# Kernel tuning notes

Hardware: AMD Instinct MI355X
Metric: run time of the kernel (lower is better)

The kernel has to match this reference:

```python
import jax, jax.numpy as jnp
import numpy as np

NUM_LANDMARKS = 256
PINV_ITERS = 6


def iterative_inv(K):
    # Newton-Schulz iterative pseudo-inverse (Nystromformer), K: [B, m, m]
    I = jnp.eye(K.shape[-1], dtype=K.dtype)
    V = K.swapaxes(-1, -2) / (jnp.max(jnp.sum(K, axis=-2)) * jnp.max(jnp.sum(K, axis=-1)))
    for _ in range(PINV_ITERS):
        KV = K @ V
        V = 0.25 * V @ (13.0 * I - KV @ (15.0 * I - KV @ (7.0 * I - KV)))
    return V


def nystrom_attention_matrix(q, k, m):
    # q, k: [B, N, d] -> approximate softmax(q k^T / sqrt(d)) of shape [B, N, N]
    B, N, d = q.shape
    scale = 1.0 / jnp.sqrt(jnp.asarray(d, q.dtype))
    L = N // m
    q_l = q.reshape(B, m, L, d).mean(axis=2)  # landmark queries [B, m, d]
    k_l = k.reshape(B, m, L, d).mean(axis=2)  # landmark keys    [B, m, d]
    k1 = jax.nn.softmax(jnp.einsum('bnd,bmd->bnm', q, k_l) * scale, axis=-1)   # [B, N, m]
    k2 = jax.nn.softmax(jnp.einsum('bld,bmd->blm', q_l, k_l) * scale, axis=-1) # [B, m, m]
    k3 = jax.nn.softmax(jnp.einsum('bmd,bnd->bmn', q_l, k) * scale, axis=-1)   # [B, m, N]
    return (k1 @ iterative_inv(k2)) @ k3  # [B, N, N]


def setup_inputs() -> dict:
    key = jax.random.key(0)
    ks = jax.random.split(key, 8)
    B, C, T, W, H = 2, 64, 4, 32, 32
    d = C // 8
    scale = 0.05  # keep q.k scores in a sane softmax range
    return {
        'x': jax.random.normal(ks[0], (B, C, T, W, H), dtype=jnp.float32),
        'wq': jax.random.normal(ks[1], (d, C), dtype=jnp.float32) * scale,
        'bq': jax.random.normal(ks[2], (d,), dtype=jnp.float32) * scale,
        'wk': jax.random.normal(ks[3], (d, C), dtype=jnp.float32) * scale,
        'bk': jax.random.normal(ks[4], (d,), dtype=jnp.float32) * scale,
        'wv': jax.random.normal(ks[5], (C, C), dtype=jnp.float32) * scale,
        'bv': jax.random.normal(ks[6], (C,), dtype=jnp.float32) * scale,
        'gamma': jax.random.normal(ks[7], (1,), dtype=jnp.float32),
    }


def reference(x, wq, bq, wk, bk, wv, bv, gamma):
    B, C, T, W, H = x.shape
    N = T * W * H
    xf = x.reshape(B, C, N)
    # 1x1x1 Conv3d == per-token linear over channels
    q = jnp.einsum('oc,bcn->bno', wq, xf) + bq            # [B, N, C//8]
    k = jnp.einsum('oc,bcn->bno', wk, xf) + bk            # [B, N, C//8]
    v = jnp.einsum('oc,bcn->bon', wv, xf) + bv[None, :, None]  # [B, C, N]
    attn = nystrom_attention_matrix(q, k, NUM_LANDMARKS)  # [B, N, N]
    # out = bmm(value, attn^T): out[b,c,i] = sum_j v[b,c,j] * attn[b,i,j]
    out = jnp.einsum('bcj,bij->bci', v, attn).reshape(B, C, T, W, H)
    out = gamma[0] * out + x
    return out, attn
```

## Files before the change

### kernel.cpp

```cpp
#include <hip/hip_runtime.h>
#include <hip/hip_bf16.h>
#include <math.h>

#define NB 2
#define NC 64
#define ND 8
#define NN 4096
#define NM 256
#define NL 16
#define SCALE 0.35355339059327373f
#define PS (NB * NM * NM)

typedef __attribute__((ext_vector_type(4))) float f32x4;
typedef __attribute__((ext_vector_type(8))) short bf16x8;

__device__ inline ushort f2bf(float f) {
  __hip_bfloat16 h = __float2bfloat16(f);
  return *reinterpret_cast<ushort*>(&h);
}
__device__ inline float bf2f(ushort u) {
  return __uint_as_float(((unsigned int)u) << 16);
}

__device__ inline void gl_lds16(const void* g, void* l) {
  __builtin_amdgcn_global_load_lds(
      (const __attribute__((address_space(1))) unsigned int*)g,
      (__attribute__((address_space(3))) unsigned int*)l, 16, 0, 0);
}

__global__ __launch_bounds__(256) void qkv2l_kernel(
    const float* __restrict__ x,
    const float* __restrict__ wq, const float* __restrict__ bq,
    const float* __restrict__ wk, const float* __restrict__ bk,
    const float* __restrict__ wv, const float* __restrict__ bv,
    float* __restrict__ q, float* __restrict__ k, float* __restrict__ v,
    float* __restrict__ ql, float* __restrict__ kl) {
  __shared__ float ws[NC];
  int o = blockIdx.x;
  int b = blockIdx.z;
  int n0 = blockIdx.y * 1024;
  int t = threadIdx.x;
  const float* wrow;
  float bias;
  if (o < ND)            { wrow = wq + (size_t)o * NC;            bias = bq[o]; }
  else if (o < 2 * ND)   { wrow = wk + (size_t)(o - ND) * NC;     bias = bk[o - ND]; }
  else                   { wrow = wv + (size_t)(o - 2 * ND) * NC; bias = bv[o - 2 * ND]; }
  if (t < NC) ws[t] = wrow[t];
  __syncthreads();
  int n = n0 + t * 4;
  float4 acc = {bias, bias, bias, bias};
  #pragma unroll
  for (int c = 0; c < NC; ++c) {
    float wc = ws[c];
    float4 xv = *(const float4*)(x + ((size_t)b * NC + c) * NN + n);
    acc.x += wc * xv.x; acc.y += wc * xv.y; acc.z += wc * xv.z; acc.w += wc * xv.w;
  }
  if (o < ND) {
    float* qp = q + ((size_t)b * NN + n) * ND + o;
    qp[0] = acc.x; qp[8] = acc.y; qp[16] = acc.z; qp[24] = acc.w;
  } else if (o < 2 * ND) {
    float* kp = k + ((size_t)b * NN + n) * ND + (o - ND);
    kp[0] = acc.x; kp[8] = acc.y; kp[16] = acc.z; kp[24] = acc.w;
  } else {
    *(float4*)(v + ((size_t)b * NC + (o - 2 * ND)) * NN + n) = acc;
  }
  if (o < 2 * ND) {
    float s4 = acc.x + acc.y + acc.z + acc.w;
    s4 += __shfl_xor(s4, 1);
    s4 += __shfl_xor(s4, 2);
    if ((t & 3) == 0) {
      int g = n0 / 16 + (t >> 2);
      float* dst = (o < ND) ? ql : kl;
      dst[((size_t)b * NM + g) * ND + (o & 7)] = s4 * (1.0f / 16.0f);
    }
  }
}

__global__ __launch_bounds__(256) void scores_all_kernel(
    const float* __restrict__ q, const float* __restrict__ ql,
    const float* __restrict__ kw, const float* __restrict__ kl,
    ushort* __restrict__ k1bf, float* __restrict__ k2w,
    float* __restrict__ k3w, float* __restrict__ kvw) {
  __shared__ float skl[NM][9];
  __shared__ float wred[4], wsum[4];
  int blk = blockIdx.x;
  int t = threadIdx.x;
  if (blk < 2048 + 128) {
    const float* Q; int R, b, xrow;
    bool isbf;
    if (blk < 2048) { b = blk >> 10; xrow = blk & 1023; Q = q;  R = NN; isbf = true; }
    else { int r = blk - 2048; b = r >> 6; xrow = r & 63; Q = ql; R = NM; isbf = false; }
    for (int i = t; i < NM * ND; i += 256) skl[i >> 3][i & 7] = kl[(size_t)b * NM * ND + i];
    __syncthreads();
    int wave = t >> 6, lane = t & 63;
    int r = xrow * 4 + wave;
    const float* qrow = Q + ((size_t)b * R + r) * ND;
    float qr[ND];
    #pragma unroll
    for (int dd = 0; dd < ND; ++dd) qr[dd] = qrow[dd];
    float sc[4];
    float lmax = -1e30f;
    #pragma unroll
    for (int s = 0; s < 4; ++s) {
      int j = lane + 64 * s;
      float a = 0.f;
      #pragma unroll
      for (int dd = 0; dd < ND; ++dd) a += qr[dd] * skl[j][dd];
      sc[s] = a * SCALE;
      lmax = fmaxf(lmax, sc[s]);
    }
    for (int off = 32; off; off >>= 1) lmax = fmaxf(lmax, __shfl_xor(lmax, off));
    float lsum = 0.f;
    #pragma unroll
    for (int s = 0; s < 4; ++s) { sc[s] = expf(sc[s] - lmax); lsum += sc[s]; }
    for (int off = 32; off; off >>= 1) lsum += __shfl_xor(lsum, off);
    float inv = 1.0f / lsum;
    if (isbf) {
      #pragma unroll
      for (int s = 0; s < 4; ++s)
        k1bf[((size_t)b * R + r) * NM + lane + 64 * s] = f2bf(sc[s] * inv);
    } else {
      #pragma unroll
      for (int s = 0; s < 4; ++s)
        k2w[((size_t)b * R + r) * NM + lane + 64 * s] = sc[s] * inv;
    }
  } else if (blk < 2048 + 128 + 512) {
    int r = blk - 2176;
    int b = r >> 8, i = r & 255;
    float qr[ND];
    #pragma unroll
    for (int dd = 0; dd < ND; ++dd) qr[dd] = ql[((size_t)b * NM + i) * ND + dd];
    float sc[16];
    float lmax = -1e30f;
    #pragma unroll
    for (int s = 0; s < 16; ++s) {
      int n = t + 256 * s;
      const float* kp = kw + ((size_t)b * NN + n) * ND;
      float a = 0.f;
      #pragma unroll
      for (int dd = 0; dd < ND; ++dd) a += qr[dd] * kp[dd];
      sc[s] = a * SCALE;
      lmax = fmaxf(lmax, sc[s]);
    }
    for (int off = 32; off; off >>= 1) lmax = fmaxf(lmax, __shfl_xor(lmax, off));
    if ((t & 63) == 0) wred[t >> 6] = lmax;
    __syncthreads();
    lmax = fmaxf(fmaxf(wred[0], wred[1]), fmaxf(wred[2], wred[3]));
    float lsum = 0.f;
    #pragma unroll
    for (int s = 0; s < 16; ++s) { sc[s] = expf(sc[s] - lmax); lsum += sc[s]; }
    for (int off = 32; off; off >>= 1) lsum += __shfl_xor(lsum, off);
    if ((t & 63) == 0) wsum[t >> 6] = lsum;
    __syncthreads();
    lsum = wsum[0] + wsum[1] + wsum[2] + wsum[3];
    float inv = 1.0f / lsum;
    #pragma unroll
    for (int s = 0; s < 16; ++s) k3w[((size_t)b * NM + i) * NN + t + 256 * s] = sc[s] * inv;
  } else {
    int r = blk - 2688;
    kvw[r * 256 + t] = 0.0f;
  }
}

__global__ __launch_bounds__(256) void denom_k3t_kernel(
    const float* __restrict__ k2, float* __restrict__ denw,
    const float* __restrict__ k3, ushort* __restrict__ k3t) {
  __shared__ float red[256];
  __shared__ float tile[32][33];
  int blk = blockIdx.x;
  int t = threadIdx.x;
  if (blk < NB) {
    int b = blk;
    float cs = 0.f;
    for (int i = 0; i < NM; ++i) cs += k2[((size_t)b * NM + i) * NM + t];
    red[t] = cs;
    __syncthreads();
    for (int off = 128; off; off >>= 1) {
      if (t < off) red[t] = fmaxf(red[t], red[t + off]);
      __syncthreads();
    }
    if (t == 0) denw[b] = red[0];
  } else {
    int r = blk - NB;
    int n0 = (r & 127) * 32, m0 = ((r >> 7) & 7) * 32, b = r >> 10;
    int rr = t >> 3, c4 = (t & 7) * 4;
    float4 v = *(const float4*)(k3 + ((size_t)b * NM + m0 + rr) * NN + n0 + c4);
    tile[c4][rr] = v.x; tile[c4 + 1][rr] = v.y; tile[c4 + 2][rr] = v.z; tile[c4 + 3][rr] = v.w;
    __syncthreads();
    ushort4 u;
    u.x = f2bf(tile[rr][c4]);     u.y = f2bf(tile[rr][c4 + 1]);
    u.z = f2bf(tile[rr][c4 + 2]); u.w = f2bf(tile[rr][c4 + 3]);
    *(ushort4*)(k3t + ((size_t)b * NN + n0 + rr) * NM + m0 + c4) = u;
  }
}

__global__ __launch_bounds__(64) void ns_gemm(
    const float* __restrict__ A, int amode,
    const float* __restrict__ B, int bmode,
    const float* __restrict__ denw, float* __restrict__ O,
    float s_a, float s_ab) {
  __shared__ float As[128][36];
  __shared__ float Bs[128][36];
  int t = threadIdx.x;
  int bj = blockIdx.x * 32, bi = blockIdx.y * 32;
  int b = blockIdx.z >> 1, slice = blockIdx.z & 1;
  int k0 = slice * 128;
  size_t bo = (size_t)b * NM * NM;
  float dval = (amode == 2 || bmode == 2) ? 1.0f / fmaxf(denw[0], denw[1]) : 0.f;
  {
    int r = t >> 1, kc0 = (t & 1) * 64;
    if (amode == 2) {
      for (int i = 0; i < 64; ++i) {
        int kk = kc0 + i;
        As[kk][r] = A[bo + (size_t)(k0 + kk) * NM + bi + r] * dval;
      }
    } else if (amode == 1) {
      for (int i = 0; i < 16; ++i) {
        const float* p = A + bo + (size_t)(bi + r) * NM + k0 + kc0 + i * 4;
        float4 v0 = *(const float4*)p;
        float4 v1 = *(const float4*)(p + PS);
        As[kc0 + i * 4 + 0][r] = v0.x + v1.x;
        As[kc0 + i * 4 + 1][r] = v0.y + v1.y;
        As[kc0 + i * 4 + 2][r] = v0.z + v1.z;
        As[kc0 + i * 4 + 3][r] = v0.w + v1.w;
      }
    } else {
      for (int i = 0; i < 16; ++i) {
        float4 v0 = *(const float4*)(A + bo + (size_t)(bi + r) * NM + k0 + kc0 + i * 4);
        As[kc0 + i * 4 + 0][r] = v0.x;
        As[kc0 + i * 4 + 1][r] = v0.y;
        As[kc0 + i * 4 + 2][r] = v0.z;
        As[kc0 + i * 4 + 3][r] = v0.w;
      }
    }
    if (bmode == 2) {
      for (int i2 = 0; i2 < 2; ++i2) {
        int kr = t + 64 * i2;
        for (int c = 0; c < 32; ++c)
          Bs[kr][c] = B[bo + (size_t)(bj + c) * NM + k0 + kr] * dval;
      }
    } else if (bmode == 1) {
      for (int i2 = 0; i2 < 2; ++i2) {
        int kr = t + 64 * i2;
        for (int c4 = 0; c4 < 32; c4 += 4) {
          const float* p = B + bo + (size_t)(k0 + kr) * NM + bj + c4;
          float4 v0 = *(const float4*)p;
          float4 v1 = *(const float4*)(p + PS);
          v0.x += v1.x; v0.y += v1.y; v0.z += v1.z; v0.w += v1.w;
          *(float4*)&Bs[kr][c4] = v0;
        }
      }
    } else {
      for (int i2 = 0; i2 < 2; ++i2) {
        int kr = t + 64 * i2;
        for (int c4 = 0; c4 < 32; c4 += 4)
          *(float4*)&Bs[kr][c4] =
              *(const float4*)(B + bo + (size_t)(k0 + kr) * NM + bj + c4);
      }
    }
  }
  __syncthreads();
  int tx = t & 7, ty = t >> 3;
  float acc[4][4] = {};
  #pragma unroll 4
  for (int kk = 0; kk < 128; ++kk) {
    float4 a4 = *(const float4*)&As[kk][ty * 4];
    float4 b4 = *(const float4*)&Bs[kk][tx * 4];
    float av[4] = {a4.x, a4.y, a4.z, a4.w};
    float bv[4] = {b4.x, b4.y, b4.z, b4.w};
    #pragma unroll
    for (int i = 0; i < 4; ++i)
      #pragma unroll
      for (int j = 0; j < 4; ++j) acc[i][j] += av[i] * bv[j];
  }
  float* Op = O + (size_t)slice * PS + bo;
  bool addA = (slice == 0) && (s_a != 0.0f);
  #pragma unroll
  for (int i = 0; i < 4; ++i) {
    int row = bi + ty * 4 + i;
    float4 rv;
    rv.x = s_ab * acc[i][0]; rv.y = s_ab * acc[i][1];
    rv.z = s_ab * acc[i][2]; rv.w = s_ab * acc[i][3];
    if (addA) {
      int col = bj + tx * 4;
      if (amode == 2) {
        rv.x += s_a * A[bo + (size_t)(col + 0) * NM + row] * dval;
        rv.y += s_a * A[bo + (size_t)(col + 1) * NM + row] * dval;
        rv.z += s_a * A[bo + (size_t)(col + 2) * NM + row] * dval;
        rv.w += s_a * A[bo + (size_t)(col + 3) * NM + row] * dval;
      } else if (amode == 1) {
        const float* p = A + bo + (size_t)row * NM + col;
        float4 a0 = *(const float4*)p;
        float4 a1 = *(const float4*)(p + PS);
        rv.x += s_a * (a0.x + a1.x); rv.y += s_a * (a0.y + a1.y);
        rv.z += s_a * (a0.z + a1.z); rv.w += s_a * (a0.w + a1.w);
      } else {
        float4 a0 = *(const float4*)(A + bo + (size_t)row * NM + col);
        rv.x += s_a * a0.x; rv.y += s_a * a0.y;
        rv.z += s_a * a0.z; rv.w += s_a * a0.w;
      }
    }
    *(float4*)(Op + (size_t)row * NM + bj + tx * 4) = rv;
  }
}

__global__ __launch_bounds__(256) void cvt_vinv_kernel(const float* __restrict__ Vp,
                                                       ushort* __restrict__ Vt) {
  int b = blockIdx.z;
  int n0 = blockIdx.x * 32, m0 = blockIdx.y * 32;
  __shared__ float tile[32][33];
  int t = threadIdx.x;
  int r = t >> 3, c4 = (t & 7) * 4;
  size_t bo = (size_t)b * NM * NM;
  const float* p = Vp + bo + (size_t)(m0 + r) * NM + n0 + c4;
  float4 v0 = *(const float4*)p;
  float4 v1 = *(const float4*)(p + PS);
  tile[c4][r] = v0.x + v1.x; tile[c4 + 1][r] = v0.y + v1.y;
  tile[c4 + 2][r] = v0.z + v1.z; tile[c4 + 3][r] = v0.w + v1.w;
  __syncthreads();
  ushort4 u;
  u.x = f2bf(tile[r][c4]);     u.y = f2bf(tile[r][c4 + 1]);
  u.z = f2bf(tile[r][c4 + 2]); u.w = f2bf(tile[r][c4 + 3]);
  *(ushort4*)(Vt + bo + (size_t)(n0 + r) * NM + m0 + c4) = u;
}

__global__ __launch_bounds__(256) void gemm_a_mfma(
    const ushort* __restrict__ k1bf, const ushort* __restrict__ Vt,
    ushort* __restrict__ Abf) {
  int b = blockIdx.z;
  int bi = blockIdx.y * 128, bj = blockIdx.x * 128;
  __shared__ ushort As[128 * 64];
  __shared__ ushort Bs[128 * 64];
  int t = threadIdx.x;
  int wave = t >> 6, lane = t & 63;
  int wr = wave >> 1, wc = wave & 1;
  const ushort* Ab = k1bf + (size_t)b * NN * NM;
  const ushort* Bb = Vt + (size_t)b * NM * NM;
  f32x4 acc[4][4] = {};
  for (int k0 = 0; k0 < NM; k0 += 64) {
    #pragma unroll
    for (int q = 0; q < 4; ++q) {
      int s = q * 256 + t;
      int r = s >> 3, c = s & 7;
      int cs = (c ^ (r & 7)) << 3;
      gl_lds16(Ab + (size_t)(bi + r) * NM + k0 + cs, As + (size_t)s * 8);
      gl_lds16(Bb + (size_t)(bj + r) * NM + k0 + cs, Bs + (size_t)s * 8);
    }
    __syncthreads();
    #pragma unroll
    for (int kk = 0; kk < 2; ++kk) {
      int koff = kk * 64 + (lane >> 4) * 16;
      bf16x8 af[4], bfv[4];
      #pragma unroll
      for (int mi = 0; mi < 4; ++mi) {
        int row = wr * 64 + mi * 16 + (lane & 15);
        af[mi] = *(const bf16x8*)((const char*)As + row * 128 + (koff ^ ((row & 7) << 4)));
      }
      #pragma unroll
      for (int nj = 0; nj < 4; ++nj) {
        int row = wc * 64 + nj * 16 + (lane & 15);
        bfv[nj] = *(const bf16x8*)((const char*)Bs + row * 128 + (koff ^ ((row & 7) << 4)));
      }
      #pragma unroll
      for (int mi = 0; mi < 4; ++mi)
        #pragma unroll
        for (int nj = 0; nj < 4; ++nj)
          acc[mi][nj] = __builtin_amdgcn_mfma_f32_16x16x32_bf16(af[mi], bfv[nj], acc[mi][nj], 0, 0, 0);
    }
    __syncthreads();
  }
  int col = lane & 15, rbase = (lane >> 4) * 4;
  #pragma unroll
  for (int mi = 0; mi < 4; ++mi)
    #pragma unroll
    for (int nj = 0; nj < 4; ++nj)
      #pragma unroll
      for (int r = 0; r < 4; ++r)
        Abf[((size_t)b * NN + bi + wr * 64 + mi * 16 + rbase + r) * NM
            + bj + wc * 64 + nj * 16 + col] = f2bf(acc[mi][nj][r]);
}

__global__ __launch_bounds__(256) void attn_kv_kernel(
    const ushort* __restrict__ Abf, const ushort* __restrict__ K3T,
    float* __restrict__ attn, const float* __restrict__ k3w,
    const float* __restrict__ vw, float* __restrict__ kvw) {
  __shared__ char smem[32768];
  int blk = blockIdx.x;
  int t = threadIdx.x;
  if (blk < 2048) {
    ushort* As = (ushort*)smem;
    ushort* Bs = (ushort*)(smem + 16384);
    int swz = (blk & 7) * 256 + (blk >> 3);
    int b = swz >> 10;
    int rem = swz & 1023;
    int bi = (rem >> 5) * 128, bj = (rem & 31) * 128;
    int wave = t >> 6, lane = t & 63;
    int wr = wave >> 1, wc = wave & 1;
    const ushort* Ab = Abf + (size_t)b * NN * NM;
    const ushort* Bb = K3T + (size_t)b * NN * NM;
    f32x4 acc[4][4] = {};
    for (int k0 = 0; k0 < NM; k0 += 64) {
      #pragma unroll
      for (int q = 0; q < 4; ++q) {
        int s = q * 256 + t;
        int r = s >> 3, c = s & 7;
        int cs = (c ^ (r & 7)) << 3;
        gl_lds16(Ab + (size_t)(bi + r) * NM + k0 + cs, As + (size_t)s * 8);
        gl_lds16(Bb + (size_t)(bj + r) * NM + k0 + cs, Bs + (size_t)s * 8);
      }
      __syncthreads();
      #pragma unroll
      for (int kk = 0; kk < 2; ++kk) {
        int koff = kk * 64 + (lane >> 4) * 16;
        bf16x8 af[4], bfv[4];
        #pragma unroll
        for (int mi = 0; mi < 4; ++mi) {
          int row = wr * 64 + mi * 16 + (lane & 15);
          af[mi] = *(const bf16x8*)((const char*)As + row * 128 + (koff ^ ((row & 7) << 4)));
        }
        #pragma unroll
        for (int nj = 0; nj < 4; ++nj) {
          int row = wc * 64 + nj * 16 + (lane & 15);
          bfv[nj] = *(const bf16x8*)((const char*)Bs + row * 128 + (koff ^ ((row & 7) << 4)));
        }
        #pragma unroll
        for (int mi = 0; mi < 4; ++mi)
          #pragma unroll
          for (int nj = 0; nj < 4; ++nj)
            acc[mi][nj] = __builtin_amdgcn_mfma_f32_16x16x32_bf16(af[mi], bfv[nj], acc[mi][nj], 0, 0, 0);
      }
      __syncthreads();
    }
    int col = lane & 15, rbase = (lane >> 4) * 4;
    #pragma unroll
    for (int mi = 0; mi < 4; ++mi)
      #pragma unroll
      for (int nj = 0; nj < 4; ++nj)
        #pragma unroll
        for (int r = 0; r < 4; ++r)
          attn[((size_t)b * NN + bi + wr * 64 + mi * 16 + rbase + r) * NN
               + bj + wc * 64 + nj * 16 + col] = acc[mi][nj][r];
  } else {
    typedef float KVRow[33];
    KVRow* Ks = (KVRow*)smem;
    KVRow* Vs = (KVRow*)(smem + 64 * 33 * 4);
    int r = blk - 2048;
    int bp = (r & 3) * 64;
    int jsl = (r >> 2) & 31;
    int b = r >> 7;
    int j0base = jsl * (NN / 32);
    int tx = t & 15, ty = t >> 4;
    int lrow = t >> 2, ljc = (t & 3) * 8;
    float acc[4][4] = {};
    for (int j0 = j0base; j0 < j0base + NN / 32; j0 += 32) {
      float4 a0 = *(const float4*)(k3w + ((size_t)b * NM + bp + lrow) * NN + j0 + ljc);
      float4 a1 = *(const float4*)(k3w + ((size_t)b * NM + bp + lrow) * NN + j0 + ljc + 4);
      float4 v0 = *(const float4*)(vw + ((size_t)b * NC + lrow) * NN + j0 + ljc);
      float4 v1 = *(const float4*)(vw + ((size_t)b * NC + lrow) * NN + j0 + ljc + 4);
      Ks[lrow][ljc + 0] = a0.x; Ks[lrow][ljc + 1] = a0.y; Ks[lrow][ljc + 2] = a0.z; Ks[lrow][ljc + 3] = a0.w;
      Ks[lrow][ljc + 4] = a1.x; Ks[lrow][ljc + 5] = a1.y; Ks[lrow][ljc + 6] = a1.z; Ks[lrow][ljc + 7] = a1.w;
      Vs[lrow][ljc + 0] = v0.x; Vs[lrow][ljc + 1] = v0.y; Vs[lrow][ljc + 2] = v0.z; Vs[lrow][ljc + 3] = v0.w;
      Vs[lrow][ljc + 4] = v1.x; Vs[lrow][ljc + 5] = v1.y; Vs[lrow][ljc + 6] = v1.z; Vs[lrow][ljc + 7] = v1.w;
      __syncthreads();
      #pragma unroll
      for (int kk = 0; kk < 32; ++kk) {
        float av_[4], bv_[4];
        #pragma unroll
        for (int i = 0; i < 4; ++i) av_[i] = Ks[(ty << 2) + i][kk];
        #pragma unroll
        for (int j = 0; j < 4; ++j) bv_[j] = Vs[(tx << 2) + j][kk];
        #pragma unroll
        for (int i = 0; i < 4; ++i)
          #pragma unroll
          for (int j = 0; j < 4; ++j) acc[i][j] += av_[i] * bv_[j];
      }
      __syncthreads();
    }
    #pragma unroll
    for (int i = 0; i < 4; ++i)
      #pragma unroll
      for (int j = 0; j < 4; ++j)
        atomicAdd(&kvw[((size_t)b * NM + bp + (ty << 2) + i) * NC + (tx << 2) + j], acc[i][j]);
  }
}

__global__ __launch_bounds__(256) void out_kernel(
    const ushort* __restrict__ Abf, const float* __restrict__ kvm,
    const float* __restrict__ x, const float* __restrict__ gamma,
    float* __restrict__ outp) {
  __shared__ float As[32 * 256];
  int blk = blockIdx.x;
  int b = blk / (NN / 32), n0 = (blk % (NN / 32)) * 32;
  int t = threadIdx.x;
  for (int it = 0; it < 32; ++it)
    As[it * 256 + (t ^ (it & 31))] = bf2f(Abf[((size_t)b * NN + n0 + it) * NM + t]);
  __syncthreads();
  int tn = t & 31, cg0 = (t >> 5) * 8;
  float g = gamma[0];
  float acc[8] = {};
  for (int p = 0; p < NM; ++p) {
    float a = As[tn * 256 + (p ^ (tn & 31))];
    float4 kv0 = *(const float4*)(kvm + ((size_t)b * NM + p) * NC + cg0);
    float4 kv1 = *(const float4*)(kvm + ((size_t)b * NM + p) * NC + cg0 + 4);
    acc[0] += a * kv0.x; acc[1] += a * kv0.y; acc[2] += a * kv0.z; acc[3] += a * kv0.w;
    acc[4] += a * kv1.x; acc[5] += a * kv1.y; acc[6] += a * kv1.z; acc[7] += a * kv1.w;
  }
  #pragma unroll
  for (int qd = 0; qd < 8; ++qd) {
    int c = cg0 + qd;
    size_t idx = ((size_t)b * NC + c) * NN + n0 + tn;
    outp[idx] = g * acc[qd] + x[idx];
  }
}

extern "C" void kernel_launch(void* const* d_in, const int* in_sizes, int n_in,
                              void* d_out, int out_size, void* d_ws, size_t ws_size,
                              hipStream_t stream) {
  const float* x     = (const float*)d_in[0];
  const float* wq    = (const float*)d_in[1];
  const float* bq    = (const float*)d_in[2];
  const float* wk    = (const float*)d_in[3];
  const float* bk    = (const float*)d_in[4];
  const float* wv    = (const float*)d_in[5];
  const float* bv    = (const float*)d_in[6];
  const float* gamma = (const float*)d_in[7];
  float* outp = (float*)d_out;
  float* attn = outp + (size_t)NB * NC * NN;
  float* w = (float*)d_ws;

  float* qw   = w;
  float* kw   = qw + 65536;
  float* vw   = kw + 65536;
  float* qlw  = vw + 524288;
  float* klw  = qlw + 4096;
  float* k1w  = klw + 4096;
  float* k2w  = k1w + 2097152;
  float* k3w  = k2w + 131072;
  float* Abuf = k3w + 2097152;
  float* Zp   = Abuf + 1048576;
  float* T1p  = Zp + 2 * PS;
  float* T2p  = T1p + 2 * PS;
  float* Vap  = T2p + 2 * PS;
  float* Vbp  = Vap + 2 * PS;
  float* kvw  = Vbp + 2 * PS;
  float* denw = kvw + 32768;
  ushort* k1bf  = (ushort*)k1w;
  ushort* k3T   = (ushort*)k1w + 2097152;
  ushort* Abf   = (ushort*)Abuf;
  ushort* Vinvt = (ushort*)Zp;

  qkv2l_kernel<<<dim3(80, NN / 1024, NB), dim3(256), 0, stream>>>(
      x, wq, bq, wk, bk, wv, bv, qw, kw, vw, qlw, klw);
  scores_all_kernel<<<dim3(2048 + 128 + 512 + 128), dim3(256), 0, stream>>>(
      qw, qlw, kw, klw, k1bf, k2w, k3w, kvw);
  denom_k3t_kernel<<<dim3(NB + 2048), dim3(256), 0, stream>>>(k2w, denw, k3w, k3T);

  const float* Vptr = k2w; int vmode = 2;
  float* Vout = Vap;
  float* Vfin = nullptr;
  for (int it = 0; it < 6; ++it) {
    ns_gemm<<<dim3(8, 8, NB * 2), dim3(64), 0, stream>>>(k2w, 0, Vptr, vmode, denw, Zp, 0.f, 1.f);
    ns_gemm<<<dim3(8, 8, NB * 2), dim3(64), 0, stream>>>(Zp, 1, Zp, 1, denw, T1p, 7.f, -1.f);
    ns_gemm<<<dim3(8, 8, NB * 2), dim3(64), 0, stream>>>(Zp, 1, T1p, 1, denw, T2p, 15.f, -1.f);
    ns_gemm<<<dim3(8, 8, NB * 2), dim3(64), 0, stream>>>(Vptr, vmode, T2p, 1, denw, Vout, 3.25f, -0.25f);
    Vfin = Vout;
    Vptr = Vout; vmode = 1;
    Vout = (Vout == Vap) ? Vbp : Vap;
  }

  cvt_vinv_kernel<<<dim3(NM / 32, NM / 32, NB), dim3(256), 0, stream>>>(Vfin, Vinvt);
  gemm_a_mfma<<<dim3(NM / 128, NN / 128, NB), dim3(256), 0, stream>>>(k1bf, Vinvt, Abf);
  attn_kv_kernel<<<dim3(2048 + 256), dim3(256), 0, stream>>>(Abf, k3T, attn, k3w, vw, kvw);
  out_kernel<<<dim3(NB * NN / 32), dim3(256), 0, stream>>>(Abf, kvw, x, gamma, outp);
}
```

Baseline: 328.8 us.

## Refactor Newton-Schulz polynomial into three GEMMs and fuse kv/out stages

Rewrites the Newton-Schulz update polynomial 13I-15KV+7KV^2-KV^3 by factoring it with a real root. This cuts the per-iteration chain from four GEMMs to three kernels, two of them independent and batched in one launch, and drops the split-K partial-sum buffers. The final iteration writes the transposed bf16 inverse directly, which removes the separate conversion kernel. The kv = k3·v^T reduction moves into the denom/transpose kernel, so the output projection can merge into the attention kernel and one launch disappears. The factored form may change floating-point rounding, and the new GEMM tiles use 256 threads with full-K loads in place of split-K.

```diff
diff --git a/kernel.cpp b/kernel.cpp
--- a/kernel.cpp
+++ b/kernel.cpp
@@ -9,7 +9,9 @@
 #define NM 256
 #define NL 16
 #define SCALE 0.35355339059327373f
-#define PS (NB * NM * NM)
+#define A_ROOT 4.1303956f
+#define B_COEF (-2.8696044f)
+#define C_COEF 3.1474086f
 
 typedef __attribute__((ext_vector_type(4))) float f32x4;
 typedef __attribute__((ext_vector_type(8))) short bf16x8;
@@ -162,14 +164,15 @@
   }
 }
 
-__global__ __launch_bounds__(256) void denom_k3t_kernel(
+__global__ __launch_bounds__(256) void denom_k3t_kv_kernel(
     const float* __restrict__ k2, float* __restrict__ denw,
-    const float* __restrict__ k3, ushort* __restrict__ k3t) {
-  __shared__ float red[256];
-  __shared__ float tile[32][33];
+    const float* __restrict__ k3, ushort* __restrict__ k3t,
+    const float* __restrict__ vw, float* __restrict__ kvw) {
+  __shared__ char smem[34048];
   int blk = blockIdx.x;
   int t = threadIdx.x;
   if (blk < NB) {
+    float* red = (float*)smem;
     int b = blk;
     float cs = 0.f;
     for (int i = 0; i < NM; ++i) cs += k2[((size_t)b * NM + i) * NM + t];
@@ -180,7 +183,9 @@
       __syncthreads();
     }
     if (t == 0) denw[b] = red[0];
-  } else {
+  } else if (blk < NB + 2048) {
+    typedef float TRow[33];
+    TRow* tile = (TRow*)smem;
     int r = blk - NB;
     int n0 = (r & 127) * 32, m0 = ((r >> 7) & 7) * 32, b = r >> 10;
     int rr = t >> 3, c4 = (t & 7) * 4;
@@ -191,137 +196,171 @@
     u.x = f2bf(tile[rr][c4]);     u.y = f2bf(tile[rr][c4 + 1]);
     u.z = f2bf(tile[rr][c4 + 2]); u.w = f2bf(tile[rr][c4 + 3]);
     *(ushort4*)(k3t + ((size_t)b * NN + n0 + rr) * NM + m0 + c4) = u;
-  }
-}
-
-__global__ __launch_bounds__(64) void ns_gemm(
+  } else {
+    typedef float KVRow[33];
+    KVRow* Ks = (KVRow*)smem;
+    KVRow* Vs = (KVRow*)(smem + 64 * 33 * 4);
+    int r = blk - (NB + 2048);
+    int bp = (r & 3) * 64;
+    int jsl = (r >> 2) & 31;
+    int b = r >> 7;
+    int j0base = jsl * (NN / 32);
+    int tx = t & 15, ty = t >> 4;
+    int lrow = t >> 2, ljc = (t & 3) * 8;
+    float acc[4][4] = {};
+    for (int j0 = j0base; j0 < j0base + NN / 32; j0 += 32) {
+      float4 a0 = *(const float4*)(k3 + ((size_t)b * NM + bp + lrow) * NN + j0 + ljc);
+      float4 a1 = *(const float4*)(k3 + ((size_t)b * NM + bp + lrow) * NN + j0 + ljc + 4);
+      float4 v0 = *(const float4*)(vw + ((size_t)b * NC + lrow) * NN + j0 + ljc);
+      float4 v1 = *(const float4*)(vw + ((size_t)b * NC + lrow) * NN + j0 + ljc + 4);
+      Ks[lrow][ljc + 0] = a0.x; Ks[lrow][ljc + 1] = a0.y; Ks[lrow][ljc + 2] = a0.z; Ks[lrow][ljc + 3] = a0.w;
+      Ks[lrow][ljc + 4] = a1.x; Ks[lrow][ljc + 5] = a1.y; Ks[lrow][ljc + 6] = a1.z; Ks[lrow][ljc + 7] = a1.w;
+      Vs[lrow][ljc + 0] = v0.x; Vs[lrow][ljc + 1] = v0.y; Vs[lrow][ljc + 2] = v0.z; Vs[lrow][ljc + 3] = v0.w;
+      Vs[lrow][ljc + 4] = v1.x; Vs[lrow][ljc + 5] = v1.y; Vs[lrow][ljc + 6] = v1.z; Vs[lrow][ljc + 7] = v1.w;
+      __syncthreads();
+      #pragma unroll
+      for (int kk = 0; kk < 32; ++kk) {
+        float av_[4], bv_[4];
+        #pragma unroll
+        for (int i = 0; i < 4; ++i) av_[i] = Ks[(ty << 2) + i][kk];
+        #pragma unroll
+        for (int j = 0; j < 4; ++j) bv_[j] = Vs[(tx << 2) + j][kk];
+        #pragma unroll
+        for (int i = 0; i < 4; ++i)
+          #pragma unroll
+          for (int j = 0; j < 4; ++j) acc[i][j] += av_[i] * bv_[j];
+      }
+      __syncthreads();
+    }
+    #pragma unroll
+    for (int i = 0; i < 4; ++i)
+      #pragma unroll
+      for (int j = 0; j < 4; ++j)
+        atomicAdd(&kvw[((size_t)b * NM + bp + (ty << 2) + i) * NC + (tx << 2) + j], acc[i][j]);
+  }
+}
+
+__device__ __forceinline__ void ns_core(
     const float* __restrict__ A, int amode,
-    const float* __restrict__ B, int bmode,
-    const float* __restrict__ denw, float* __restrict__ O,
-    float s_a, float s_ab) {
-  __shared__ float As[128][36];
-  __shared__ float Bs[128][36];
-  int t = threadIdx.x;
-  int bj = blockIdx.x * 32, bi = blockIdx.y * 32;
-  int b = blockIdx.z >> 1, slice = blockIdx.z & 1;
-  int k0 = slice * 128;
+    const float* __restrict__ B, int bmode, const float* __restrict__ Bp,
+    float dval, float s_a, float s_ab,
+    float* __restrict__ O, ushort* __restrict__ Ot, int wmode,
+    int bi, int bj, size_t bo, float (*As)[260], float (*Bs)[36], int t) {
+  if (amode == 0) {
+    #pragma unroll
+    for (int q = 0; q < 8; ++q) {
+      int s = q * 256 + t;
+      int r = s >> 6, kc = (s & 63) * 4;
+      *(float4*)&As[r][kc] = *(const float4*)(A + bo + (size_t)(bi + r) * NM + kc);
+    }
+  } else {
+    #pragma unroll
+    for (int q = 0; q < 8; ++q) {
+      int s = q * 256 + t;
+      int k = s >> 3, rc = (s & 7) * 4;
+      float4 v = *(const float4*)(A + bo + (size_t)k * NM + bi + rc);
+      As[rc + 0][k] = v.x * dval; As[rc + 1][k] = v.y * dval;
+      As[rc + 2][k] = v.z * dval; As[rc + 3][k] = v.w * dval;
+    }
+  }
+  if (bmode == 0) {
+    #pragma unroll
+    for (int q = 0; q < 8; ++q) {
+      int s = q * 256 + t;
+      int k = s >> 3, c = (s & 7) * 4;
+      *(float4*)&Bs[k][c] = *(const float4*)(B + bo + (size_t)k * NM + bj + c);
+    }
+  } else if (bmode == 2) {
+    #pragma unroll
+    for (int q = 0; q < 8; ++q) {
+      int s = q * 256 + t;
+      int c = s >> 6, k4 = (s & 63) * 4;
+      float4 v = *(const float4*)(B + bo + (size_t)(bj + c) * NM + k4);
+      Bs[k4 + 0][c] = v.x * dval; Bs[k4 + 1][c] = v.y * dval;
+      Bs[k4 + 2][c] = v.z * dval; Bs[k4 + 3][c] = v.w * dval;
+    }
+  } else {
+    #pragma unroll
+    for (int q = 0; q < 8; ++q) {
+      int s = q * 256 + t;
+      int k = s >> 3, c = (s & 7) * 4;
+      float4 v = *(const float4*)(B + bo + (size_t)k * NM + bj + c);
+      float4 z = *(const float4*)(Bp + bo + (size_t)k * NM + bj + c);
+      float4 rr;
+      rr.x = v.x + B_COEF * z.x; rr.y = v.y + B_COEF * z.y;
+      rr.z = v.z + B_COEF * z.z; rr.w = v.w + B_COEF * z.w;
+      int d = k - bj - c;
+      if (d >= 0 && d < 4) ((float*)&rr)[d] += C_COEF;
+      *(float4*)&Bs[k][c] = rr;
+    }
+  }
+  __syncthreads();
+  int tx = t & 15, ty = t >> 4;
+  float acc[2][2] = {};
+  #pragma unroll 8
+  for (int kk = 0; kk < NM; ++kk) {
+    float a0 = As[ty * 2][kk], a1 = As[ty * 2 + 1][kk];
+    float b0 = Bs[kk][tx * 2], b1 = Bs[kk][tx * 2 + 1];
+    acc[0][0] += a0 * b0; acc[0][1] += a0 * b1;
+    acc[1][0] += a1 * b0; acc[1][1] += a1 * b1;
+  }
+  #pragma unroll
+  for (int i = 0; i < 2; ++i)
+    #pragma unroll
+    for (int j = 0; j < 2; ++j) {
+      int R = bi + ty * 2 + i, C = bj + tx * 2 + j;
+      float rv = s_ab * acc[i][j];
+      if (s_a != 0.0f) {
+        float av;
+        if (amode == 2) av = A[bo + (size_t)C * NM + R] * dval;
+        else            av = A[bo + (size_t)R * NM + C];
+        rv += s_a * av;
+      }
+      if (wmode == 0) O[bo + (size_t)R * NM + C] = rv;
+      else            Ot[bo + (size_t)C * NM + R] = f2bf(rv);
+    }
+}
+
+__global__ __launch_bounds__(256) void ns_z_kernel(
+    const float* __restrict__ k2, const float* __restrict__ V, int bmode,
+    const float* __restrict__ denw, float* __restrict__ Z) {
+  __shared__ float As[32][260];
+  __shared__ float Bs[256][36];
+  int bj = blockIdx.x * 32, bi = blockIdx.y * 32, b = blockIdx.z;
   size_t bo = (size_t)b * NM * NM;
-  float dval = (amode == 2 || bmode == 2) ? 1.0f / fmaxf(denw[0], denw[1]) : 0.f;
-  {
-    int r = t >> 1, kc0 = (t & 1) * 64;
-    if (amode == 2) {
-      for (int i = 0; i < 64; ++i) {
-        int kk = kc0 + i;
-        As[kk][r] = A[bo + (size_t)(k0 + kk) * NM + bi + r] * dval;
-      }
-    } else if (amode == 1) {
-      for (int i = 0; i < 16; ++i) {
-        const float* p = A + bo + (size_t)(bi + r) * NM + k0 + kc0 + i * 4;
-        float4 v0 = *(const float4*)p;
-        float4 v1 = *(const float4*)(p + PS);
-        As[kc0 + i * 4 + 0][r] = v0.x + v1.x;
-        As[kc0 + i * 4 + 1][r] = v0.y + v1.y;
-        As[kc0 + i * 4 + 2][r] = v0.z + v1.z;
-        As[kc0 + i * 4 + 3][r] = v0.w + v1.w;
-      }
-    } else {
-      for (int i = 0; i < 16; ++i) {
-        float4 v0 = *(const float4*)(A + bo + (size_t)(bi + r) * NM + k0 + kc0 + i * 4);
-        As[kc0 + i * 4 + 0][r] = v0.x;
-        As[kc0 + i * 4 + 1][r] = v0.y;
-        As[kc0 + i * 4 + 2][r] = v0.z;
-        As[kc0 + i * 4 + 3][r] = v0.w;
-      }
-    }
-    if (bmode == 2) {
-      for (int i2 = 0; i2 < 2; ++i2) {
-        int kr = t + 64 * i2;
-        for (int c = 0; c < 32; ++c)
-          Bs[kr][c] = B[bo + (size_t)(bj + c) * NM + k0 + kr] * dval;
-      }
-    } else if (bmode == 1) {
-      for (int i2 = 0; i2 < 2; ++i2) {
-        int kr = t + 64 * i2;
-        for (int c4 = 0; c4 < 32; c4 += 4) {
-          const float* p = B + bo + (size_t)(k0 + kr) * NM + bj + c4;
-          float4 v0 = *(const float4*)p;
-          float4 v1 = *(const float4*)(p + PS);
-          v0.x += v1.x; v0.y += v1.y; v0.z += v1.z; v0.w += v1.w;
-          *(float4*)&Bs[kr][c4] = v0;
-        }
-      }
-    } else {
-      for (int i2 = 0; i2 < 2; ++i2) {
-        int kr = t + 64 * i2;
-        for (int c4 = 0; c4 < 32; c4 += 4)
-          *(float4*)&Bs[kr][c4] =
-              *(const float4*)(B + bo + (size_t)(k0 + kr) * NM + bj + c4);
-      }
-    }
-  }
-  __syncthreads();
-  int tx = t & 7, ty = t >> 3;
-  float acc[4][4] = {};
-  #pragma unroll 4
-  for (int kk = 0; kk < 128; ++kk) {
-    float4 a4 = *(const float4*)&As[kk][ty * 4];
-    float4 b4 = *(const float4*)&Bs[kk][tx * 4];
-    float av[4] = {a4.x, a4.y, a4.z, a4.w};
-    float bv[4] = {b4.x, b4.y, b4.z, b4.w};
-    #pragma unroll
-    for (int i = 0; i < 4; ++i)
-      #pragma unroll
-      for (int j = 0; j < 4; ++j) acc[i][j] += av[i] * bv[j];
-  }
-  float* Op = O + (size_t)slice * PS + bo;
-  bool addA = (slice == 0) && (s_a != 0.0f);
-  #pragma unroll
-  for (int i = 0; i < 4; ++i) {
-    int row = bi + ty * 4 + i;
-    float4 rv;
-    rv.x = s_ab * acc[i][0]; rv.y = s_ab * acc[i][1];
-    rv.z = s_ab * acc[i][2]; rv.w = s_ab * acc[i][3];
-    if (addA) {
-      int col = bj + tx * 4;
-      if (amode == 2) {
-        rv.x += s_a * A[bo + (size_t)(col + 0) * NM + row] * dval;
-        rv.y += s_a * A[bo + (size_t)(col + 1) * NM + row] * dval;
-        rv.z += s_a * A[bo + (size_t)(col + 2) * NM + row] * dval;
-        rv.w += s_a * A[bo + (size_t)(col + 3) * NM + row] * dval;
-      } else if (amode == 1) {
-        const float* p = A + bo + (size_t)row * NM + col;
-        float4 a0 = *(const float4*)p;
-        float4 a1 = *(const float4*)(p + PS);
-        rv.x += s_a * (a0.x + a1.x); rv.y += s_a * (a0.y + a1.y);
-        rv.z += s_a * (a0.z + a1.z); rv.w += s_a * (a0.w + a1.w);
-      } else {
-        float4 a0 = *(const float4*)(A + bo + (size_t)row * NM + col);
-        rv.x += s_a * a0.x; rv.y += s_a * a0.y;
-        rv.z += s_a * a0.z; rv.w += s_a * a0.w;
-      }
-    }
-    *(float4*)(Op + (size_t)row * NM + bj + tx * 4) = rv;
-  }
-}
-
-__global__ __launch_bounds__(256) void cvt_vinv_kernel(const float* __restrict__ Vp,
-                                                       ushort* __restrict__ Vt) {
-  int b = blockIdx.z;
-  int n0 = blockIdx.x * 32, m0 = blockIdx.y * 32;
-  __shared__ float tile[32][33];
-  int t = threadIdx.x;
-  int r = t >> 3, c4 = (t & 7) * 4;
+  float dval = (bmode == 2) ? 1.0f / fmaxf(denw[0], denw[1]) : 0.f;
+  ns_core(k2, 0, (bmode == 2) ? k2 : V, bmode, nullptr, dval, 0.f, 1.f,
+          Z, nullptr, 0, bi, bj, bo, As, Bs, threadIdx.x);
+}
+
+__global__ __launch_bounds__(256) void ns_uz2_kernel(
+    const float* __restrict__ Vc, int amode, const float* __restrict__ Z,
+    const float* __restrict__ denw, float* __restrict__ U, float* __restrict__ Z2) {
+  __shared__ float As[32][260];
+  __shared__ float Bs[256][36];
+  int bj = blockIdx.x * 32, bi = blockIdx.y * 32, z = blockIdx.z;
+  if (z < NB) {
+    size_t bo = (size_t)z * NM * NM;
+    float dval = (amode == 2) ? 1.0f / fmaxf(denw[0], denw[1]) : 0.f;
+    ns_core(Vc, amode, Z, 0, nullptr, dval, -A_ROOT, 1.f,
+            U, nullptr, 0, bi, bj, bo, As, Bs, threadIdx.x);
+  } else {
+    size_t bo = (size_t)(z - NB) * NM * NM;
+    ns_core(Z, 0, Z, 0, nullptr, 0.f, 0.f, 1.f,
+            Z2, nullptr, 0, bi, bj, bo, As, Bs, threadIdx.x);
+  }
+}
+
+__global__ __launch_bounds__(256) void ns_v_kernel(
+    const float* __restrict__ U, const float* __restrict__ Z2,
+    const float* __restrict__ Z, float* __restrict__ Vout,
+    ushort* __restrict__ Vinvt, int wmode) {
+  __shared__ float As[32][260];
+  __shared__ float Bs[256][36];
+  int bj = blockIdx.x * 32, bi = blockIdx.y * 32, b = blockIdx.z;
   size_t bo = (size_t)b * NM * NM;
-  const float* p = Vp + bo + (size_t)(m0 + r) * NM + n0 + c4;
-  float4 v0 = *(const float4*)p;
-  float4 v1 = *(const float4*)(p + PS);
-  tile[c4][r] = v0.x + v1.x; tile[c4 + 1][r] = v0.y + v1.y;
-  tile[c4 + 2][r] = v0.z + v1.z; tile[c4 + 3][r] = v0.w + v1.w;
-  __syncthreads();
-  ushort4 u;
-  u.x = f2bf(tile[r][c4]);     u.y = f2bf(tile[r][c4 + 1]);
-  u.z = f2bf(tile[r][c4 + 2]); u.w = f2bf(tile[r][c4 + 3]);
-  *(ushort4*)(Vt + bo + (size_t)(n0 + r) * NM + m0 + c4) = u;
+  ns_core(U, 0, Z2, 3, Z, 0.f, 0.f, -0.25f,
+          Vout, Vinvt, wmode, bi, bj, bo, As, Bs, threadIdx.x);
 }
 
 __global__ __launch_bounds__(256) void gemm_a_mfma(
@@ -380,10 +419,11 @@
             + bj + wc * 64 + nj * 16 + col] = f2bf(acc[mi][nj][r]);
 }
 
-__global__ __launch_bounds__(256) void attn_kv_kernel(
+__global__ __launch_bounds__(256) void attn_out_kernel(
     const ushort* __restrict__ Abf, const ushort* __restrict__ K3T,
-    float* __restrict__ attn, const float* __restrict__ k3w,
-    const float* __restrict__ vw, float* __restrict__ kvw) {
+    float* __restrict__ attn, const float* __restrict__ kvm,
+    const float* __restrict__ x, const float* __restrict__ gamma,
+    float* __restrict__ outp) {
   __shared__ char smem[32768];
   int blk = blockIdx.x;
   int t = threadIdx.x;
@@ -441,75 +481,28 @@
           attn[((size_t)b * NN + bi + wr * 64 + mi * 16 + rbase + r) * NN
                + bj + wc * 64 + nj * 16 + col] = acc[mi][nj][r];
   } else {
-    typedef float KVRow[33];
-    KVRow* Ks = (KVRow*)smem;
-    KVRow* Vs = (KVRow*)(smem + 64 * 33 * 4);
+    float* Asf = (float*)smem;
     int r = blk - 2048;
-    int bp = (r & 3) * 64;
-    int jsl = (r >> 2) & 31;
-    int b = r >> 7;
-    int j0base = jsl * (NN / 32);
-    int tx = t & 15, ty = t >> 4;
-    int lrow = t >> 2, ljc = (t & 3) * 8;
-    float acc[4][4] = {};
-    for (int j0 = j0base; j0 < j0base + NN / 32; j0 += 32) {
-      float4 a0 = *(const float4*)(k3w + ((size_t)b * NM + bp + lrow) * NN + j0 + ljc);
-      float4 a1 = *(const float4*)(k3w + ((size_t)b * NM + bp + lrow) * NN + j0 + ljc + 4);
-      float4 v0 = *(const float4*)(vw + ((size_t)b * NC + lrow) * NN + j0 + ljc);
-      float4 v1 = *(const float4*)(vw + ((size_t)b * NC + lrow) * NN + j0 + ljc + 4);
-      Ks[lrow][ljc + 0] = a0.x; Ks[lrow][ljc + 1] = a0.y; Ks[lrow][ljc + 2] = a0.z; Ks[lrow][ljc + 3] = a0.w;
-      Ks[lrow][ljc + 4] = a1.x; Ks[lrow][ljc + 5] = a1.y; Ks[lrow][ljc + 6] = a1.z; Ks[lrow][ljc + 7] = a1.w;
-      Vs[lrow][ljc + 0] = v0.x; Vs[lrow][ljc + 1] = v0.y; Vs[lrow][ljc + 2] = v0.z; Vs[lrow][ljc + 3] = v0.w;
-      Vs[lrow][ljc + 4] = v1.x; Vs[lrow][ljc + 5] = v1.y; Vs[lrow][ljc + 6] = v1.z; Vs[lrow][ljc + 7] = v1.w;
-      __syncthreads();
-      #pragma unroll
-      for (int kk = 0; kk < 32; ++kk) {
-        float av_[4], bv_[4];
-        #pragma unroll
-        for (int i = 0; i < 4; ++i) av_[i] = Ks[(ty << 2) + i][kk];
-        #pragma unroll
-        for (int j = 0; j < 4; ++j) bv_[j] = Vs[(tx << 2) + j][kk];
-        #pragma unroll
-        for (int i = 0; i < 4; ++i)
-          #pragma unroll
-          for (int j = 0; j < 4; ++j) acc[i][j] += av_[i] * bv_[j];
-      }
-      __syncthreads();
-    }
-    #pragma unroll
-    for (int i = 0; i < 4; ++i)
-      #pragma unroll
-      for (int j = 0; j < 4; ++j)
-        atomicAdd(&kvw[((size_t)b * NM + bp + (ty << 2) + i) * NC + (tx << 2) + j], acc[i][j]);
-  }
-}
-
-__global__ __launch_bounds__(256) void out_kernel(
-    const ushort* __restrict__ Abf, const float* __restrict__ kvm,
-    const float* __restrict__ x, const float* __restrict__ gamma,
-    float* __restrict__ outp) {
-  __shared__ float As[32 * 256];
-  int blk = blockIdx.x;
-  int b = blk / (NN / 32), n0 = (blk % (NN / 32)) * 32;
-  int t = threadIdx.x;
-  for (int it = 0; it < 32; ++it)
-    As[it * 256 + (t ^ (it & 31))] = bf2f(Abf[((size_t)b * NN + n0 + it) * NM + t]);
-  __syncthreads();
-  int tn = t & 31, cg0 = (t >> 5) * 8;
-  float g = gamma[0];
-  float acc[8] = {};
-  for (int p = 0; p < NM; ++p) {
-    float a = As[tn * 256 + (p ^ (tn & 31))];
-    float4 kv0 = *(const float4*)(kvm + ((size_t)b * NM + p) * NC + cg0);
-    float4 kv1 = *(const float4*)(kvm + ((size_t)b * NM + p) * NC + cg0 + 4);
-    acc[0] += a * kv0.x; acc[1] += a * kv0.y; acc[2] += a * kv0.z; acc[3] += a * kv0.w;
-    acc[4] += a * kv1.x; acc[5] += a * kv1.y; acc[6] += a * kv1.z; acc[7] += a * kv1.w;
-  }
-  #pragma unroll
-  for (int qd = 0; qd < 8; ++qd) {
-    int c = cg0 + qd;
-    size_t idx = ((size_t)b * NC + c) * NN + n0 + tn;
-    outp[idx] = g * acc[qd] + x[idx];
+    int b = r >> 7, n0 = (r & 127) * 32;
+    for (int it = 0; it < 32; ++it)
+      Asf[it * 256 + (t ^ (it & 31))] = bf2f(Abf[((size_t)b * NN + n0 + it) * NM + t]);
+    __syncthreads();
+    int tn = t & 31, cg0 = (t >> 5) * 8;
+    float g = gamma[0];
+    float acc[8] = {};
+    for (int p = 0; p < NM; ++p) {
+      float a = Asf[tn * 256 + (p ^ (tn & 31))];
+      float4 kv0 = *(const float4*)(kvm + ((size_t)b * NM + p) * NC + cg0);
+      float4 kv1 = *(const float4*)(kvm + ((size_t)b * NM + p) * NC + cg0 + 4);
+      acc[0] += a * kv0.x; acc[1] += a * kv0.y; acc[2] += a * kv0.z; acc[3] += a * kv0.w;
+      acc[4] += a * kv1.x; acc[5] += a * kv1.y; acc[6] += a * kv1.z; acc[7] += a * kv1.w;
+    }
+    #pragma unroll
+    for (int qd = 0; qd < 8; ++qd) {
+      int c = cg0 + qd;
+      size_t idx = ((size_t)b * NC + c) * NN + n0 + tn;
+      outp[idx] = g * acc[qd] + x[idx];
+    }
   }
 }
 
@@ -537,39 +530,35 @@
   float* k2w  = k1w + 2097152;
   float* k3w  = k2w + 131072;
   float* Abuf = k3w + 2097152;
-  float* Zp   = Abuf + 1048576;
-  float* T1p  = Zp + 2 * PS;
-  float* T2p  = T1p + 2 * PS;
-  float* Vap  = T2p + 2 * PS;
-  float* Vbp  = Vap + 2 * PS;
-  float* kvw  = Vbp + 2 * PS;
+  float* Zb   = Abuf + 1048576;
+  float* Z2b  = Zb + 131072;
+  float* Ub   = Z2b + 131072;
+  float* Vab  = Ub + 131072;
+  float* Vtw  = Vab + 131072;
+  float* kvw  = Vtw + 65536;
   float* denw = kvw + 32768;
   ushort* k1bf  = (ushort*)k1w;
   ushort* k3T   = (ushort*)k1w + 2097152;
   ushort* Abf   = (ushort*)Abuf;
-  ushort* Vinvt = (ushort*)Zp;
+  ushort* Vinvt = (ushort*)Vtw;
 
   qkv2l_kernel<<<dim3(80, NN / 1024, NB), dim3(256), 0, stream>>>(
       x, wq, bq, wk, bk, wv, bv, qw, kw, vw, qlw, klw);
   scores_all_kernel<<<dim3(2048 + 128 + 512 + 128), dim3(256), 0, stream>>>(
       qw, qlw, kw, klw, k1bf, k2w, k3w, kvw);
-  denom_k3t_kernel<<<dim3(NB + 2048), dim3(256), 0, stream>>>(k2w, denw, k3w, k3T);
-
-  const float* Vptr = k2w; int vmode = 2;
-  float* Vout = Vap;
-  float* Vfin = nullptr;
+  denom_k3t_kv_kernel<<<dim3(NB + 2048 + 256), dim3(256), 0, stream>>>(
+      k2w, denw, k3w, k3T, vw, kvw);
+
   for (int it = 0; it < 6; ++it) {
-    ns_gemm<<<dim3(8, 8, NB * 2), dim3(64), 0, stream>>>(k2w, 0, Vptr, vmode, denw, Zp, 0.f, 1.f);
-    ns_gemm<<<dim3(8, 8, NB * 2), dim3(64), 0, stream>>>(Zp, 1, Zp, 1, denw, T1p, 7.f, -1.f);
-    ns_gemm<<<dim3(8, 8, NB * 2), dim3(64), 0, stream>>>(Zp, 1, T1p, 1, denw, T2p, 15.f, -1.f);
-    ns_gemm<<<dim3(8, 8, NB * 2), dim3(64), 0, stream>>>(Vptr, vmode, T2p, 1, denw, Vout, 3.25f, -0.25f);
-    Vfin = Vout;
-    Vptr = Vout; vmode = 1;
-    Vout = (Vout == Vap) ? Vbp : Vap;
-  }
-
-  cvt_vinv_kernel<<<dim3(NM / 32, NM / 32, NB), dim3(256), 0, stream>>>(Vfin, Vinvt);
+    int vm = (it == 0) ? 2 : 0;
+    ns_z_kernel<<<dim3(8, 8, NB), dim3(256), 0, stream>>>(k2w, Vab, vm, denw, Zb);
+    ns_uz2_kernel<<<dim3(8, 8, 2 * NB), dim3(256), 0, stream>>>(
+        (it == 0) ? k2w : Vab, vm, Zb, denw, Ub, Z2b);
+    ns_v_kernel<<<dim3(8, 8, NB), dim3(256), 0, stream>>>(
+        Ub, Z2b, Zb, Vab, Vinvt, (it == 5) ? 1 : 0);
+  }
+
   gemm_a_mfma<<<dim3(NM / 128, NN / 128, NB), dim3(256), 0, stream>>>(k1bf, Vinvt, Abf);
-  attn_kv_kernel<<<dim3(2048 + 256), dim3(256), 0, stream>>>(Abf, k3T, attn, k3w, vw, kvw);
-  out_kernel<<<dim3(NB * NN / 32), dim3(256), 0, stream>>>(Abf, kvw, x, gamma, outp);
-}
+  attn_out_kernel<<<dim3(2048 + 256), dim3(256), 0, stream>>>(
+      Abf, k3T, attn, kvw, x, gamma, outp);
+}
```

New measurement: 334.5 us. No clear change (+1.7%).
